# Kernel optimization log

Hardware: AMD Instinct MI355X
Metric: run time of the kernel (lower is better)

The kernel has to match this reference:

```python
import jax, jax.numpy as jnp
import numpy as np

N = 100000
E = 1600000
D = 64


def setup_inputs() -> dict:
    key = jax.random.key(0)
    ks = jax.random.split(key, 10)
    x = jax.random.normal(ks[0], (N, D), dtype=jnp.float32)
    edge_index = jax.random.randint(ks[1], (2, E), 0, N, dtype=jnp.int64)
    edge_weight = jax.random.uniform(ks[2], (E,), dtype=jnp.float32)
    s = 1.0 / np.sqrt(D)
    # GraphConv params: lin_rel (with bias) applied to aggregated messages,
    # lin_root (no bias) applied to the node's own features.
    W_rel1 = jax.random.uniform(ks[3], (D, D), jnp.float32, -s, s)
    b_rel1 = jax.random.uniform(ks[4], (D,), jnp.float32, -s, s)
    W_root1 = jax.random.uniform(ks[5], (D, D), jnp.float32, -s, s)
    W_rel2 = jax.random.uniform(ks[6], (D, D), jnp.float32, -s, s)
    b_rel2 = jax.random.uniform(ks[7], (D,), jnp.float32, -s, s)
    W_root2 = jax.random.uniform(ks[8], (D, D), jnp.float32, -s, s)
    return {"x": x, "edge_index": edge_index, "edge_weight": edge_weight,
            "W_rel1": W_rel1, "b_rel1": b_rel1, "W_root1": W_root1,
            "W_rel2": W_rel2, "b_rel2": b_rel2, "W_root2": W_root2}


def _graph_conv(x, src, dst, ew, W_rel, b_rel, W_root):
    # message: x_j * e_ji, scatter-add at target node i (edge_index[1])
    msg = x[src] * ew[:, None]                                   # [E, D]
    agg = jax.ops.segment_sum(msg, dst, num_segments=x.shape[0])  # [N, D]
    return agg @ W_rel.T + b_rel + x @ W_root.T


def reference(x, edge_index, edge_weight, W_rel1, b_rel1, W_root1, W_rel2, b_rel2, W_root2):
    src, dst = edge_index[0], edge_index[1]
    h = _graph_conv(x, src, dst, edge_weight, W_rel1, b_rel1, W_root1)
    h = jax.nn.relu(h)
    h = _graph_conv(h, src, dst, edge_weight, W_rel2, b_rel2, W_root2)
    return h  # final ReLU dropped (layers[:-1])
```

## Files before the change

kernel.cpp:

```cpp
#include <hip/hip_runtime.h>
#include <hip/hip_bf16.h>
#include <stdint.h>


#define D 64
#define SCAN_CHUNK 1024
#define EPB   4096
#define NBMAX 256
#define CAPB  10240

typedef unsigned int   u32;
typedef unsigned short u16;

__device__ __forceinline__ float bf2f(u16 v) {
    return __uint_as_float(((u32)v) << 16);
}
__device__ __forceinline__ u16 f2bf(float f) {
    u32 u = __float_as_uint(f);
    u32 r = (u + 0x7fffu + ((u >> 16) & 1u)) >> 16;
    return (u16)r;
}

__global__ __launch_bounds__(512) void binA_kernel(
    const int* __restrict__ ei, const float* __restrict__ ew,
    int* __restrict__ deg, int* __restrict__ bucketCnt,
    uint64_t* __restrict__ bucketBuf, int E_, int nb)
{
    __shared__ uint64_t lds_e[EPB];
    __shared__ int lcnt[NBMAX];
    __shared__ int loff[NBMAX];
    __shared__ int gbase[NBMAX];

    int tid  = threadIdx.x;
    int tile = blockIdx.x * EPB;
    int cnt  = min(EPB, E_ - tile);
    if (cnt <= 0) return;

    for (int k = tid; k < nb; k += 512) lcnt[k] = 0;
    __syncthreads();

    bool     val[8];
    int      lp[8], bk[8];
    uint64_t ent[8];
#pragma unroll
    for (int j = 0; j < 8; ++j) {
        int l = j * 512 + tid;
        val[j] = (l < cnt);
        if (val[j]) {
            int e   = tile + l;
            int src = ei[e];
            int dst = ei[E_ + e];
            atomicAdd(&deg[dst], 1);
            u32 wb  = (u32)f2bf(ew[e]) & 0x7FFFu;
            u32 p32 = ((u32)src << 15) | wb;
            int b   = dst >> 9;
            ent[j] = ((uint64_t)(u32)dst << 32) | p32;
            bk[j]  = b;
            lp[j]  = atomicAdd(&lcnt[b], 1);
        }
    }
    __syncthreads();

    if (tid == 0) {
        int run = 0;
        for (int b = 0; b < nb; ++b) { int c = lcnt[b]; loff[b] = run; run += c; }
    }
    __syncthreads();
    if (tid < nb) gbase[tid] = atomicAdd(&bucketCnt[tid], lcnt[tid]);
    __syncthreads();

#pragma unroll
    for (int j = 0; j < 8; ++j)
        if (val[j]) lds_e[loff[bk[j]] + lp[j]] = ent[j];
    __syncthreads();

    for (int k = tid; k < cnt; k += 512) {
        uint64_t en = lds_e[k];
        int b   = (int)(en >> 41);
        int gp  = gbase[b] + (k - loff[b]);
        if (gp < CAPB)
            bucketBuf[(size_t)b * CAPB + gp] = en;
    }
}

__global__ __launch_bounds__(256) void scan1_kernel(
    const int* __restrict__ deg, int* __restrict__ loc, int* __restrict__ partial, int n)
{
    __shared__ int wsum[4];
    int t = threadIdx.x;
    int base = blockIdx.x * SCAN_CHUNK + t * 4;
    int v0 = (base + 0 < n) ? deg[base + 0] : 0;
    int v1 = (base + 1 < n) ? deg[base + 1] : 0;
    int v2 = (base + 2 < n) ? deg[base + 2] : 0;
    int v3 = (base + 3 < n) ? deg[base + 3] : 0;
    int s = v0 + v1 + v2 + v3;
    int lane = t & 63, wave = t >> 6;
    int inc = s;
    for (int off = 1; off < 64; off <<= 1) {
        int u = __shfl_up(inc, off);
        if (lane >= off) inc += u;
    }
    if (lane == 63) wsum[wave] = inc;
    __syncthreads();
    int woff = 0;
    for (int w = 0; w < wave; ++w) woff += wsum[w];
    int ex = woff + inc - s;
    if (base + 0 < n) loc[base + 0] = ex;
    if (base + 1 < n) loc[base + 1] = ex + v0;
    if (base + 2 < n) loc[base + 2] = ex + v0 + v1;
    if (base + 3 < n) loc[base + 3] = ex + v0 + v1 + v2;
    if (t == 255) partial[blockIdx.x] = woff + inc;
}

__global__ __launch_bounds__(1024) void scan2_kernel(int* __restrict__ partial, int nchunk)
{
    __shared__ int sd[1024];
    int t = threadIdx.x;
    if (t < nchunk) sd[t] = partial[t];
    __syncthreads();
    if (t == 0) {
        int run = 0;
        for (int i = 0; i < nchunk; ++i) { int v = sd[i]; sd[i] = run; run += v; }
    }
    __syncthreads();
    if (t < nchunk) partial[t] = sd[t];
}

__global__ __launch_bounds__(256) void scan3_kernel(
    int* __restrict__ rowptr, const int* __restrict__ partial,
    int* __restrict__ cursor, int n, int Etot)
{
    int i = blockIdx.x * 256 + threadIdx.x;
    if (i == 0) rowptr[n] = Etot;
    if (i >= n) return;
    int v = rowptr[i] + partial[i >> 10];
    rowptr[i] = v;
    cursor[i] = v;
}

__global__ __launch_bounds__(256) void binB_kernel(
    const uint64_t* __restrict__ bucketBuf, const int* __restrict__ bucketCnt,
    const int* __restrict__ rowptr, u32* __restrict__ pairs, int nb, int Nn)
{
    __shared__ int lcur[512];
    int b = blockIdx.x;
    if (b >= nb) return;
    int node0 = b << 9;
    int tid = threadIdx.x;
    for (int k = tid; k < 512; k += 256)
        lcur[k] = (node0 + k < Nn) ? rowptr[node0 + k] : 0;
    __syncthreads();

    int cnt = min(bucketCnt[b], CAPB);
    for (int k = tid; k < cnt; k += 256) {
        uint64_t en = bucketBuf[(size_t)b * CAPB + k];
        int dst = (int)(en >> 32);
        int p = atomicAdd(&lcur[dst - node0], 1);
        pairs[p] = (u32)en;
    }
}

#define GW 8
#define GR 4
__global__ __launch_bounds__(512) void gemm_kernel(
    const float* xin,
    const float* __restrict__ Wrel, const float* __restrict__ brel,
    const float* __restrict__ Wroot,
    u16* __restrict__ xr, float* io, int Nn)
{
    __shared__ float WrelT[D][D + 1];
    __shared__ float WrootT[D][D + 1];
    __shared__ float bias[D];
    __shared__ float rowX[GW][GR][D];

    int tid = threadIdx.x;
    for (int i = tid; i < D * D; i += 512) {
        int d = i >> 6, k = i & 63;
        WrelT [k][d] = Wrel [i];
        WrootT[k][d] = Wroot[i];
    }
    if (tid < D) bias[tid] = brel[tid];
    __syncthreads();

    int wave = tid >> 6, lane = tid & 63;

    int base = (blockIdx.x * GW + wave) * GR;
    if (base >= Nn) return;
    int nr = min(GR, Nn - base);

    for (int r = 0; r < nr; ++r)
        rowX[wave][r][lane] = xin[(size_t)(base + r) * D + lane];

    float aR[GR] = {0.f, 0.f, 0.f, 0.f};
    float aC[GR] = {0.f, 0.f, 0.f, 0.f};
#pragma unroll
    for (int k4 = 0; k4 < 16; ++k4) {
        float4 xv[GR];
#pragma unroll
        for (int r = 0; r < GR; ++r)
            xv[r] = *reinterpret_cast<const float4*>(&rowX[wave][r][k4 * 4]);
#pragma unroll
        for (int kk = 0; kk < 4; ++kk) {
            float wr = WrelT [k4 * 4 + kk][lane];
            float wc = WrootT[k4 * 4 + kk][lane];
#pragma unroll
            for (int r = 0; r < GR; ++r) {
                float xk = (kk == 0) ? xv[r].x : (kk == 1) ? xv[r].y
                         : (kk == 2) ? xv[r].z : xv[r].w;
                aR[r] = fmaf(xk, wr, aR[r]);
                aC[r] = fmaf(xk, wc, aC[r]);
            }
        }
    }
    for (int r = 0; r < nr; ++r) {
        size_t o = (size_t)(base + r) * D + lane;
        xr[o] = f2bf(aR[r]);
        io[o] = aC[r] + bias[lane];
    }
}

__global__ __launch_bounds__(512) void gather1_fused(
    const u16* __restrict__ xr1, const u32* __restrict__ pairs,
    const int* __restrict__ rowptr,
    const float* __restrict__ Wrel, const float* __restrict__ brel,
    const float* __restrict__ Wroot,
    u16* __restrict__ xr2, float* __restrict__ io, int Nn)
{
    __shared__ float WrelT[D][D + 1];
    __shared__ float WrootT[D][D + 1];
    __shared__ float bias[D];
    __shared__ float rowH[GW][2][D];

    int tid = threadIdx.x;
    for (int i2 = tid; i2 < D * D; i2 += 512) {
        int d = i2 >> 6, k = i2 & 63;
        WrelT [k][d] = Wrel [i2];
        WrootT[k][d] = Wroot[i2];
    }
    if (tid < D) bias[tid] = brel[tid];
    __syncthreads();

    int wave = tid >> 6, lane = tid & 63;
    int i0 = ((int)blockIdx.x * GW + wave) * 2;
    if (i0 >= Nn) return;
    int i1 = i0 + 1;
    bool row1v = (i1 < Nn);
    int i1c = row1v ? i1 : i0;

    int beg0 = __builtin_amdgcn_readfirstlane(rowptr[i0]);
    int end0 = __builtin_amdgcn_readfirstlane(rowptr[i0 + 1]);
    int beg1 = __builtin_amdgcn_readfirstlane(rowptr[i1c]);
    int end1 = __builtin_amdgcn_readfirstlane(rowptr[i1c + 1]);
    int deg0 = end0 - beg0;
    int deg1 = row1v ? (end1 - beg1) : 0;
    int dmax = max(deg0, deg1);

    int half = lane >> 5;
    int c    = lane & 31;

    float a00 = 0.f, a01 = 0.f, a10 = 0.f, a11 = 0.f;
    for (int b = 0; b < dmax; b += 16) {
#pragma unroll
        for (int jj = 0; jj < 8; ++jj) {
            int j0 = b + 2 * jj;
            u32 q0 = pairs[beg0 + j0];
            u32 q1 = pairs[beg0 + j0 + 1];
            int   s00 = (j0     < deg0) ? (int)(q0 >> 15) : 0;
            float w00 = (j0     < deg0) ? __uint_as_float((q0 & 0x7FFFu) << 16) : 0.f;
            int   s01 = (j0 + 1 < deg0) ? (int)(q1 >> 15) : 0;
            float w01 = (j0 + 1 < deg0) ? __uint_as_float((q1 & 0x7FFFu) << 16) : 0.f;
            int   sa  = half ? s01 : s00;
            float wa  = half ? w01 : w00;
            u32 va = *reinterpret_cast<const u32*>(xr1 + (size_t)sa * D + c * 2);
            u32 r0 = pairs[beg1 + j0];
            u32 r1 = pairs[beg1 + j0 + 1];
            int   s10 = (j0     < deg1) ? (int)(r0 >> 15) : 0;
            float w10 = (j0     < deg1) ? __uint_as_float((r0 & 0x7FFFu) << 16) : 0.f;
            int   s11 = (j0 + 1 < deg1) ? (int)(r1 >> 15) : 0;
            float w11 = (j0 + 1 < deg1) ? __uint_as_float((r1 & 0x7FFFu) << 16) : 0.f;
            int   sb  = half ? s11 : s10;
            float wb  = half ? w11 : w10;
            u32 vb = *reinterpret_cast<const u32*>(xr1 + (size_t)sb * D + c * 2);

            a00 = fmaf(__uint_as_float(va << 16),          wa, a00);
            a01 = fmaf(__uint_as_float(va & 0xFFFF0000u),  wa, a01);
            a10 = fmaf(__uint_as_float(vb << 16),          wb, a10);
            a11 = fmaf(__uint_as_float(vb & 0xFFFF0000u),  wb, a11);
        }
    }
    a00 += __shfl_xor(a00, 32);
    a01 += __shfl_xor(a01, 32);
    a10 += __shfl_xor(a10, 32);
    a11 += __shfl_xor(a11, 32);

    if (lane < 32) {
        *reinterpret_cast<float2*>(&rowH[wave][0][c * 2]) = make_float2(a00, a01);
        *reinterpret_cast<float2*>(&rowH[wave][1][c * 2]) = make_float2(a10, a11);
    }

    size_t o0 = (size_t)i0 * D + lane;
    float h0 = fmaxf(rowH[wave][0][lane] + io[o0], 0.f);
    rowH[wave][0][lane] = h0;
    size_t o1 = (size_t)i1c * D + lane;
    float h1 = fmaxf(rowH[wave][1][lane] + io[o1], 0.f);
    rowH[wave][1][lane] = h1;

#pragma unroll
    for (int r = 0; r < 2; ++r) {
        if (r == 1 && !row1v) break;
        const float4* rH4 = reinterpret_cast<const float4*>(rowH[wave][r]);
        float aR = 0.f;
        float aC = bias[lane];
#pragma unroll
        for (int k4 = 0; k4 < 16; ++k4) {
            float4 hv = rH4[k4];
            int k = k4 * 4;
            aR = fmaf(hv.x, WrelT [k + 0][lane], aR);
            aR = fmaf(hv.y, WrelT [k + 1][lane], aR);
            aR = fmaf(hv.z, WrelT [k + 2][lane], aR);
            aR = fmaf(hv.w, WrelT [k + 3][lane], aR);
            aC = fmaf(hv.x, WrootT[k + 0][lane], aC);
            aC = fmaf(hv.y, WrootT[k + 1][lane], aC);
            aC = fmaf(hv.z, WrootT[k + 2][lane], aC);
            aC = fmaf(hv.w, WrootT[k + 3][lane], aC);
        }
        size_t o = (size_t)(i0 + r) * D + lane;
        xr2[o] = f2bf(aR);
        io[o]  = aC;
    }
}

#define AW 8
__global__ __launch_bounds__(512) void gather2_kernel(
    const u16* __restrict__ xr, const u32* __restrict__ pairs,
    const int* __restrict__ rowptr, float* __restrict__ io, int Nn)
{
    int tid  = threadIdx.x;
    int wave = tid >> 6, lane = tid & 63;
    int i0 = ((int)blockIdx.x * AW + wave) * 2;
    if (i0 >= Nn) return;
    int i1 = i0 + 1;
    bool row1v = (i1 < Nn);
    int i1c = row1v ? i1 : i0;

    int beg0 = __builtin_amdgcn_readfirstlane(rowptr[i0]);
    int end0 = __builtin_amdgcn_readfirstlane(rowptr[i0 + 1]);
    int beg1 = __builtin_amdgcn_readfirstlane(rowptr[i1c]);
    int end1 = __builtin_amdgcn_readfirstlane(rowptr[i1c + 1]);
    int deg0 = end0 - beg0;
    int deg1 = row1v ? (end1 - beg1) : 0;
    int dmax = max(deg0, deg1);

    int half = lane >> 5;
    int c    = lane & 31;

    float a00 = 0.f, a01 = 0.f, a10 = 0.f, a11 = 0.f;
    for (int b = 0; b < dmax; b += 16) {
#pragma unroll
        for (int jj = 0; jj < 8; ++jj) {
            int j0 = b + 2 * jj;
            u32 q0 = pairs[beg0 + j0];
            u32 q1 = pairs[beg0 + j0 + 1];
            int   s00 = (j0     < deg0) ? (int)(q0 >> 15) : 0;
            float w00 = (j0     < deg0) ? __uint_as_float((q0 & 0x7FFFu) << 16) : 0.f;
            int   s01 = (j0 + 1 < deg0) ? (int)(q1 >> 15) : 0;
            float w01 = (j0 + 1 < deg0) ? __uint_as_float((q1 & 0x7FFFu) << 16) : 0.f;
            int   sa  = half ? s01 : s00;
            float wa  = half ? w01 : w00;
            u32 va = *reinterpret_cast<const u32*>(xr + (size_t)sa * D + c * 2);
            u32 r0 = pairs[beg1 + j0];
            u32 r1 = pairs[beg1 + j0 + 1];
            int   s10 = (j0     < deg1) ? (int)(r0 >> 15) : 0;
            float w10 = (j0     < deg1) ? __uint_as_float((r0 & 0x7FFFu) << 16) : 0.f;
            int   s11 = (j0 + 1 < deg1) ? (int)(r1 >> 15) : 0;
            float w11 = (j0 + 1 < deg1) ? __uint_as_float((r1 & 0x7FFFu) << 16) : 0.f;
            int   sb  = half ? s11 : s10;
            float wb  = half ? w11 : w10;
            u32 vb = *reinterpret_cast<const u32*>(xr + (size_t)sb * D + c * 2);

            a00 = fmaf(__uint_as_float(va << 16),         wa, a00);
            a01 = fmaf(__uint_as_float(va & 0xFFFF0000u), wa, a01);
            a10 = fmaf(__uint_as_float(vb << 16),         wb, a10);
            a11 = fmaf(__uint_as_float(vb & 0xFFFF0000u), wb, a11);
        }
    }
    a00 += __shfl_xor(a00, 32);
    a01 += __shfl_xor(a01, 32);
    a10 += __shfl_xor(a10, 32);
    a11 += __shfl_xor(a11, 32);

    if (lane < 32) {
        float2* p0 = reinterpret_cast<float2*>(&io[(size_t)i0 * D + c * 2]);
        float2 c0 = *p0; c0.x += a00; c0.y += a01; *p0 = c0;
        if (row1v) {
            float2* p1 = reinterpret_cast<float2*>(&io[(size_t)i1 * D + c * 2]);
            float2 c1 = *p1; c1.x += a10; c1.y += a11; *p1 = c1;
        }
    }
}

extern "C" void kernel_launch(void* const* d_in, const int* in_sizes, int n_in,
                              void* d_out, int out_size, void* d_ws, size_t ws_size,
                              hipStream_t stream)
{
    const float* x      = (const float*)d_in[0];
    const int*   ei     = (const int*)  d_in[1];
    const float* ew     = (const float*)d_in[2];
    const float* Wrel1  = (const float*)d_in[3];
    const float* brel1  = (const float*)d_in[4];
    const float* Wroot1 = (const float*)d_in[5];
    const float* Wrel2  = (const float*)d_in[6];
    const float* brel2  = (const float*)d_in[7];
    const float* Wroot2 = (const float*)d_in[8];
    float* out = (float*)d_out;

    const int E_ = in_sizes[2];
    const int Nn = in_sizes[0] / D;
    const int nb = (Nn + 511) >> 9;

    char* w = (char*)d_ws;
    size_t off = 0;
    u16*  xr1    = (u16*)(w + off); off += (size_t)Nn * D * sizeof(u16);
    u16*  xr2    = (u16*)(w + off); off += (size_t)Nn * D * sizeof(u16);
    uint64_t* bucketBuf = (uint64_t*)d_ws;
    int*  rowptr = (int*)(w + off); off += (size_t)(Nn + 1) * sizeof(int);
    int*  cursor = (int*)(w + off); off += (size_t)Nn * sizeof(int);
    int*  bucketCnt = (int*)(w + off); off += NBMAX * sizeof(int);
    int*  partial= (int*)(w + off); off += 1024 * sizeof(int);
    off = (off + 15) & ~(size_t)15;
    u32* pairs = (u32*)(w + off);

    const int nchunk  = (Nn + SCAN_CHUNK - 1) / SCAN_CHUNK;
    const int aBlocks = (E_ + EPB - 1) / EPB;
    const int gemmBlocks = (Nn + GW * GR - 1) / (GW * GR);
    const int g1Blocks   = (Nn + GW * 2 - 1) / (GW * 2);
    const int g2Blocks   = (Nn + AW * 2 - 1) / (AW * 2);

    (void)hipMemsetAsync(cursor, 0, ((size_t)Nn + NBMAX) * sizeof(int), stream);
    binA_kernel<<<aBlocks, 512, 0, stream>>>(ei, ew, cursor, bucketCnt, bucketBuf, E_, nb);
    scan1_kernel<<<nchunk, 256, 0, stream>>>(cursor, rowptr, partial, Nn);
    scan2_kernel<<<1, 1024, 0, stream>>>(partial, nchunk);
    scan3_kernel<<<(Nn + 255) / 256, 256, 0, stream>>>(rowptr, partial, cursor, Nn, E_);
    binB_kernel<<<nb, 256, 0, stream>>>(bucketBuf, bucketCnt, rowptr, pairs, nb, Nn);

    gemm_kernel<<<gemmBlocks, 512, 0, stream>>>(x, Wrel1, brel1, Wroot1, xr1, out, Nn);
    gather1_fused<<<g1Blocks, 512, 0, stream>>>(xr1, pairs, rowptr,
                                                Wrel2, brel2, Wroot2, xr2, out, Nn);
    gather2_kernel<<<g2Blocks, 512, 0, stream>>>(xr2, pairs, rowptr, out, Nn);
}
```

Before: 281.4 us.

## Unfuse layer-2 GEMM from first gather; reuse a templated gather plus separate GEMM

Removes the fused gather+ReLU+GEMM kernel and instead runs a templated gather kernel that applies ReLU in its epilogue, followed by the existing GEMM kernel on the intermediate features and then the non-ReLU gather. The goal is to free the gather from the large shared-memory weight tiles and per-block weight loading, which should raise occupancy for the latency-bound edge gather. The cost is an extra full round trip of the fp32 hidden activations through global memory and one more kernel launch. The GEMM now reads and writes the same buffer in place, which relies on each block reading its rows before writing them.

Measured after the change: 286.0 us. Within noise of the previous version (+1.6%).

```diff
diff --git a/kernel.cpp b/kernel.cpp
--- a/kernel.cpp
+++ b/kernel.cpp
@@ -219,119 +219,9 @@
     }
 }
 
-__global__ __launch_bounds__(512) void gather1_fused(
-    const u16* __restrict__ xr1, const u32* __restrict__ pairs,
-    const int* __restrict__ rowptr,
-    const float* __restrict__ Wrel, const float* __restrict__ brel,
-    const float* __restrict__ Wroot,
-    u16* __restrict__ xr2, float* __restrict__ io, int Nn)
-{
-    __shared__ float WrelT[D][D + 1];
-    __shared__ float WrootT[D][D + 1];
-    __shared__ float bias[D];
-    __shared__ float rowH[GW][2][D];
-
-    int tid = threadIdx.x;
-    for (int i2 = tid; i2 < D * D; i2 += 512) {
-        int d = i2 >> 6, k = i2 & 63;
-        WrelT [k][d] = Wrel [i2];
-        WrootT[k][d] = Wroot[i2];
-    }
-    if (tid < D) bias[tid] = brel[tid];
-    __syncthreads();
-
-    int wave = tid >> 6, lane = tid & 63;
-    int i0 = ((int)blockIdx.x * GW + wave) * 2;
-    if (i0 >= Nn) return;
-    int i1 = i0 + 1;
-    bool row1v = (i1 < Nn);
-    int i1c = row1v ? i1 : i0;
-
-    int beg0 = __builtin_amdgcn_readfirstlane(rowptr[i0]);
-    int end0 = __builtin_amdgcn_readfirstlane(rowptr[i0 + 1]);
-    int beg1 = __builtin_amdgcn_readfirstlane(rowptr[i1c]);
-    int end1 = __builtin_amdgcn_readfirstlane(rowptr[i1c + 1]);
-    int deg0 = end0 - beg0;
-    int deg1 = row1v ? (end1 - beg1) : 0;
-    int dmax = max(deg0, deg1);
-
-    int half = lane >> 5;
-    int c    = lane & 31;
-
-    float a00 = 0.f, a01 = 0.f, a10 = 0.f, a11 = 0.f;
-    for (int b = 0; b < dmax; b += 16) {
-#pragma unroll
-        for (int jj = 0; jj < 8; ++jj) {
-            int j0 = b + 2 * jj;
-            u32 q0 = pairs[beg0 + j0];
-            u32 q1 = pairs[beg0 + j0 + 1];
-            int   s00 = (j0     < deg0) ? (int)(q0 >> 15) : 0;
-            float w00 = (j0     < deg0) ? __uint_as_float((q0 & 0x7FFFu) << 16) : 0.f;
-            int   s01 = (j0 + 1 < deg0) ? (int)(q1 >> 15) : 0;
-            float w01 = (j0 + 1 < deg0) ? __uint_as_float((q1 & 0x7FFFu) << 16) : 0.f;
-            int   sa  = half ? s01 : s00;
-            float wa  = half ? w01 : w00;
-            u32 va = *reinterpret_cast<const u32*>(xr1 + (size_t)sa * D + c * 2);
-            u32 r0 = pairs[beg1 + j0];
-            u32 r1 = pairs[beg1 + j0 + 1];
-            int   s10 = (j0     < deg1) ? (int)(r0 >> 15) : 0;
-            float w10 = (j0     < deg1) ? __uint_as_float((r0 & 0x7FFFu) << 16) : 0.f;
-            int   s11 = (j0 + 1 < deg1) ? (int)(r1 >> 15) : 0;
-            float w11 = (j0 + 1 < deg1) ? __uint_as_float((r1 & 0x7FFFu) << 16) : 0.f;
-            int   sb  = half ? s11 : s10;
-            float wb  = half ? w11 : w10;
-            u32 vb = *reinterpret_cast<const u32*>(xr1 + (size_t)sb * D + c * 2);
-
-            a00 = fmaf(__uint_as_float(va << 16),          wa, a00);
-            a01 = fmaf(__uint_as_float(va & 0xFFFF0000u),  wa, a01);
-            a10 = fmaf(__uint_as_float(vb << 16),          wb, a10);
-            a11 = fmaf(__uint_as_float(vb & 0xFFFF0000u),  wb, a11);
-        }
-    }
-    a00 += __shfl_xor(a00, 32);
-    a01 += __shfl_xor(a01, 32);
-    a10 += __shfl_xor(a10, 32);
-    a11 += __shfl_xor(a11, 32);
-
-    if (lane < 32) {
-        *reinterpret_cast<float2*>(&rowH[wave][0][c * 2]) = make_float2(a00, a01);
-        *reinterpret_cast<float2*>(&rowH[wave][1][c * 2]) = make_float2(a10, a11);
-    }
-
-    size_t o0 = (size_t)i0 * D + lane;
-    float h0 = fmaxf(rowH[wave][0][lane] + io[o0], 0.f);
-    rowH[wave][0][lane] = h0;
-    size_t o1 = (size_t)i1c * D + lane;
-    float h1 = fmaxf(rowH[wave][1][lane] + io[o1], 0.f);
-    rowH[wave][1][lane] = h1;
-
-#pragma unroll
-    for (int r = 0; r < 2; ++r) {
-        if (r == 1 && !row1v) break;
-        const float4* rH4 = reinterpret_cast<const float4*>(rowH[wave][r]);
-        float aR = 0.f;
-        float aC = bias[lane];
-#pragma unroll
-        for (int k4 = 0; k4 < 16; ++k4) {
-            float4 hv = rH4[k4];
-            int k = k4 * 4;
-            aR = fmaf(hv.x, WrelT [k + 0][lane], aR);
-            aR = fmaf(hv.y, WrelT [k + 1][lane], aR);
-            aR = fmaf(hv.z, WrelT [k + 2][lane], aR);
-            aR = fmaf(hv.w, WrelT [k + 3][lane], aR);
-            aC = fmaf(hv.x, WrootT[k + 0][lane], aC);
-            aC = fmaf(hv.y, WrootT[k + 1][lane], aC);
-            aC = fmaf(hv.z, WrootT[k + 2][lane], aC);
-            aC = fmaf(hv.w, WrootT[k + 3][lane], aC);
-        }
-        size_t o = (size_t)(i0 + r) * D + lane;
-        xr2[o] = f2bf(aR);
-        io[o]  = aC;
-    }
-}
-
 #define AW 8
-__global__ __launch_bounds__(512) void gather2_kernel(
+template <bool RELU>
+__global__ __launch_bounds__(512) void gather_kernel(
     const u16* __restrict__ xr, const u32* __restrict__ pairs,
     const int* __restrict__ rowptr, float* __restrict__ io, int Nn)
 {
@@ -391,10 +281,16 @@
 
     if (lane < 32) {
         float2* p0 = reinterpret_cast<float2*>(&io[(size_t)i0 * D + c * 2]);
-        float2 c0 = *p0; c0.x += a00; c0.y += a01; *p0 = c0;
+        float2 c0 = *p0;
+        c0.x += a00; c0.y += a01;
+        if (RELU) { c0.x = fmaxf(c0.x, 0.f); c0.y = fmaxf(c0.y, 0.f); }
+        *p0 = c0;
         if (row1v) {
             float2* p1 = reinterpret_cast<float2*>(&io[(size_t)i1 * D + c * 2]);
-            float2 c1 = *p1; c1.x += a10; c1.y += a11; *p1 = c1;
+            float2 c1 = *p1;
+            c1.x += a10; c1.y += a11;
+            if (RELU) { c1.x = fmaxf(c1.x, 0.f); c1.y = fmaxf(c1.y, 0.f); }
+            *p1 = c1;
         }
     }
 }
@@ -433,8 +329,7 @@
     const int nchunk  = (Nn + SCAN_CHUNK - 1) / SCAN_CHUNK;
     const int aBlocks = (E_ + EPB - 1) / EPB;
     const int gemmBlocks = (Nn + GW * GR - 1) / (GW * GR);
-    const int g1Blocks   = (Nn + GW * 2 - 1) / (GW * 2);
-    const int g2Blocks   = (Nn + AW * 2 - 1) / (AW * 2);
+    const int gBlocks    = (Nn + AW * 2 - 1) / (AW * 2);
 
     (void)hipMemsetAsync(cursor, 0, ((size_t)Nn + NBMAX) * sizeof(int), stream);
     binA_kernel<<<aBlocks, 512, 0, stream>>>(ei, ew, cursor, bucketCnt, bucketBuf, E_, nb);
@@ -444,7 +339,8 @@
     binB_kernel<<<nb, 256, 0, stream>>>(bucketBuf, bucketCnt, rowptr, pairs, nb, Nn);
 
     gemm_kernel<<<gemmBlocks, 512, 0, stream>>>(x, Wrel1, brel1, Wroot1, xr1, out, Nn);
-    gather1_fused<<<g1Blocks, 512, 0, stream>>>(xr1, pairs, rowptr,
-                                                Wrel2, brel2, Wroot2, xr2, out, Nn);
-    gather2_kernel<<<g2Blocks, 512, 0, stream>>>(xr2, pairs, rowptr, out, Nn);
-}
+    gather_kernel<true><<<gBlocks, 512, 0, stream>>>(xr1, pairs, rowptr, out, Nn);
+
+    gemm_kernel<<<gemmBlocks, 512, 0, stream>>>(out, Wrel2, brel2, Wroot2, xr2, out, Nn);
+    gather_kernel<false><<<gBlocks, 512, 0, stream>>>(xr2, pairs, rowptr, out, Nn);
+}
```

## Replace global degree atomics with per-bucket LDS degree counting kernel

Applied to the files above, without the earlier changes.

Removes the per-edge global atomicAdd on the degree array from the binning kernel. Degrees are now computed in a new kernel that rereads each bucket and counts in shared memory, writing the degree array directly, so the memset shrinks to the bucket counters only. Edges per block are halved (EPB 2048, 4 per thread), giving more binning blocks. The cost is an extra launch plus a second read of the bucket buffer.

Measured after the change: 242.5 us. 1.16x faster.

```diff
diff --git a/kernel.cpp b/kernel.cpp
--- a/kernel.cpp
+++ b/kernel.cpp
@@ -5,9 +5,13 @@
 
 #define D 64
 #define SCAN_CHUNK 1024
-#define EPB   4096
+#define EPB   2048
+#define EPT   4
 #define NBMAX 256
 #define CAPB  10240
+#define GW 8
+#define GR 4
+#define AW 8
 
 typedef unsigned int   u32;
 typedef unsigned short u16;
@@ -23,8 +27,7 @@
 
 __global__ __launch_bounds__(512) void binA_kernel(
     const int* __restrict__ ei, const float* __restrict__ ew,
-    int* __restrict__ deg, int* __restrict__ bucketCnt,
-    uint64_t* __restrict__ bucketBuf, int E_, int nb)
+    int* __restrict__ bucketCnt, uint64_t* __restrict__ bucketBuf, int E_, int nb)
 {
     __shared__ uint64_t lds_e[EPB];
     __shared__ int lcnt[NBMAX];
@@ -39,18 +42,17 @@
     for (int k = tid; k < nb; k += 512) lcnt[k] = 0;
     __syncthreads();
 
-    bool     val[8];
-    int      lp[8], bk[8];
-    uint64_t ent[8];
-#pragma unroll
-    for (int j = 0; j < 8; ++j) {
+    bool     val[EPT];
+    int      lp[EPT], bk[EPT];
+    uint64_t ent[EPT];
+#pragma unroll
+    for (int j = 0; j < EPT; ++j) {
         int l = j * 512 + tid;
         val[j] = (l < cnt);
         if (val[j]) {
             int e   = tile + l;
             int src = ei[e];
             int dst = ei[E_ + e];
-            atomicAdd(&deg[dst], 1);
             u32 wb  = (u32)f2bf(ew[e]) & 0x7FFFu;
             u32 p32 = ((u32)src << 15) | wb;
             int b   = dst >> 9;
@@ -70,7 +72,7 @@
     __syncthreads();
 
 #pragma unroll
-    for (int j = 0; j < 8; ++j)
+    for (int j = 0; j < EPT; ++j)
         if (val[j]) lds_e[loff[bk[j]] + lp[j]] = ent[j];
     __syncthreads();
 
@@ -81,6 +83,28 @@
         if (gp < CAPB)
             bucketBuf[(size_t)b * CAPB + gp] = en;
     }
+}
+
+__global__ __launch_bounds__(256) void degB_kernel(
+    const uint64_t* __restrict__ bucketBuf, const int* __restrict__ bucketCnt,
+    int* __restrict__ deg, int nb, int Nn)
+{
+    __shared__ int ldeg[512];
+    int b = blockIdx.x;
+    if (b >= nb) return;
+    int node0 = b << 9;
+    int tid = threadIdx.x;
+    for (int k = tid; k < 512; k += 256) ldeg[k] = 0;
+    __syncthreads();
+
+    int cnt = min(bucketCnt[b], CAPB);
+    for (int k = tid; k < cnt; k += 256) {
+        uint64_t en = bucketBuf[(size_t)b * CAPB + k];
+        atomicAdd(&ldeg[((int)(en >> 32)) - node0], 1);
+    }
+    __syncthreads();
+    for (int k = tid; k < 512; k += 256)
+        if (node0 + k < Nn) deg[node0 + k] = ldeg[k];
 }
 
 __global__ __launch_bounds__(256) void scan1_kernel(
@@ -160,8 +184,6 @@
     }
 }
 
-#define GW 8
-#define GR 4
 __global__ __launch_bounds__(512) void gemm_kernel(
     const float* xin,
     const float* __restrict__ Wrel, const float* __restrict__ brel,
@@ -330,7 +352,6 @@
     }
 }
 
-#define AW 8
 __global__ __launch_bounds__(512) void gather2_kernel(
     const u16* __restrict__ xr, const u32* __restrict__ pairs,
     const int* __restrict__ rowptr, float* __restrict__ io, int Nn)
@@ -436,8 +457,9 @@
     const int g1Blocks   = (Nn + GW * 2 - 1) / (GW * 2);
     const int g2Blocks   = (Nn + AW * 2 - 1) / (AW * 2);
 
-    (void)hipMemsetAsync(cursor, 0, ((size_t)Nn + NBMAX) * sizeof(int), stream);
-    binA_kernel<<<aBlocks, 512, 0, stream>>>(ei, ew, cursor, bucketCnt, bucketBuf, E_, nb);
+    (void)hipMemsetAsync(bucketCnt, 0, NBMAX * sizeof(int), stream);
+    binA_kernel<<<aBlocks, 512, 0, stream>>>(ei, ew, bucketCnt, bucketBuf, E_, nb);
+    degB_kernel<<<nb, 256, 0, stream>>>(bucketBuf, bucketCnt, cursor, nb, Nn);
     scan1_kernel<<<nchunk, 256, 0, stream>>>(cursor, rowptr, partial, Nn);
     scan2_kernel<<<1, 1024, 0, stream>>>(partial, nchunk);
     scan3_kernel<<<(Nn + 255) / 256, 256, 0, stream>>>(rowptr, partial, cursor, Nn, E_);
```
